# Performance work log

Measured on AMD Instinct MI355X. Metric: run time of the kernel, lower is better.

## Reference

```python
import jax, jax.numpy as jnp
import numpy as np

THETA = 10.0  # gaussian sharpness from __init__


def _bilinear_align_corners(x, out_h, out_w):
    # torch F.interpolate(mode='bilinear', align_corners=True)
    n, c, H, W = x.shape
    ys = jnp.arange(out_h, dtype=x.dtype) * ((H - 1) / (out_h - 1))
    xs = jnp.arange(out_w, dtype=x.dtype) * ((W - 1) / (out_w - 1))
    y0 = jnp.floor(ys).astype(jnp.int32)
    y1 = jnp.minimum(y0 + 1, H - 1)
    wy = ys - y0.astype(x.dtype)
    x0 = jnp.floor(xs).astype(jnp.int32)
    x1 = jnp.minimum(x0 + 1, W - 1)
    wx = xs - x0.astype(x.dtype)
    top = x[:, :, y0, :]
    bot = x[:, :, y1, :]
    xh = top * (1 - wy)[None, None, :, None] + bot * wy[None, None, :, None]
    left = xh[:, :, :, x0]
    right = xh[:, :, :, x1]
    return left * (1 - wx)[None, None, None, :] + right * wx[None, None, None, :]


def _unfold3x3(x):
    # torch F.unfold(kernel_size=3, padding=1, stride=1).view(n, c, 9, h, w)
    # zero padding; kernel positions in row-major order
    n, c, h, w = x.shape
    p = jnp.pad(x, ((0, 0), (0, 0), (1, 1), (1, 1)))
    patches = [p[:, :, di:di + h, dj:dj + w] for di in range(3) for dj in range(3)]
    return jnp.stack(patches, axis=2)  # [n, c, 9, h, w]


def reference(mask, edge):
    n, c, h, w = mask.shape
    e = _bilinear_align_corners(edge, h, w)          # [n, 1, h, w]
    le = e[:, :, None] - _unfold3x3(e)               # [n, 1, 9, h, w]
    wgt = jax.nn.softmax(-THETA * le * le, axis=2)   # gaussian similarity softmax over 3x3 nbhd
    m = _unfold3x3(mask) * wgt                       # [n, c, 9, h, w]
    return m.sum(axis=2)                             # [n, c, h, w]


def setup_inputs() -> dict:
    key = jax.random.key(0)
    k1, k2 = jax.random.split(key)
    mask = jax.random.normal(k1, (8, 64, 128, 128), dtype=jnp.float32)
    edge = jax.random.normal(k2, (8, 1, 64, 64), dtype=jnp.float32)
    return {"mask": mask, "edge": edge}
```

## Files before the change

### kernel.cpp

```cpp
#include <hip/hip_runtime.h>


#define THETA 10.0f

constexpr int NB = 8;
constexpr int C  = 64;
constexpr int H  = 128, W = 128;
constexpr int EH = 64,  EW = 64;

constexpr int ROWS = 8;
constexpr int CG   = 8;

typedef float f4v __attribute__((ext_vector_type(4)));

__global__ __launch_bounds__(256) void geg_kernel(
    const float* __restrict__ mask,
    const float* __restrict__ edge,
    float* __restrict__ out)
{
    __shared__ float e_s[ROWS + 2][W + 4];

    const int t     = threadIdx.x;
    const int cg    = blockIdx.x;
    const int ytile = blockIdx.y;
    const int n     = blockIdx.z;
    const int y0    = ytile * ROWS;

    const int lane = t & 31;
    const int x4   = lane * 4;
    const int r    = t >> 5;
    const int gy   = y0 + r;

    int rowoff[3];
    rowoff[0] = max(gy - 1, 0) * W + x4;
    rowoff[1] = gy * W + x4;
    rowoff[2] = min(gy + 1, H - 1) * W + x4;

    const int c0 = cg * CG;
    const float* mptr = mask + (size_t)(n * C + c0) * (H * W);

    float4 buf[2][3];
    #pragma unroll
    for (int i = 0; i < 3; ++i) {
        buf[0][i] = *(const float4*)(mptr + rowoff[i]);
        buf[1][i] = *(const float4*)(mptr + H * W + rowoff[i]);
    }

    const float* eg = edge + n * (EH * EW);
    const float s = 63.0f / 127.0f;
    const int rr0 = t >> 7;
    const int cc0 = t & 127;
    #pragma unroll
    for (int rb = 0; rb < ROWS + 2; rb += 2) {
        const int rr = rb + rr0;
        for (int cc = cc0; cc < W + 2; cc += 128) {
            int egy = y0 - 1 + rr;
            int egx = cc - 1;
            float v = 0.0f;
            if (egy >= 0 && egy < H && egx >= 0 && egx < W) {
                float ys = egy * s;
                float xs = egx * s;
                float yf = floorf(ys), xf = floorf(xs);
                int iy0 = (int)yf, ix0 = (int)xf;
                int iy1 = min(iy0 + 1, EH - 1), ix1 = min(ix0 + 1, EW - 1);
                float wy = ys - yf, wx = xs - xf;
                float tl = eg[iy0 * EW + ix0], tr = eg[iy0 * EW + ix1];
                float bl = eg[iy1 * EW + ix0], br = eg[iy1 * EW + ix1];
                float lv = tl + (bl - tl) * wy;
                float rv = tr + (br - tr) * wy;
                v = lv + (rv - lv) * wx;
            }
            e_s[rr][cc] = v;
        }
    }
    __syncthreads();

    float w[4][9];
    #pragma unroll
    for (int p = 0; p < 4; ++p) {
        const int gx = x4 + p;
        const float c = e_s[r + 1][gx + 1];
        float a[9], sum = 0.0f;
        #pragma unroll
        for (int di = 0; di < 3; ++di) {
            #pragma unroll
            for (int dj = 0; dj < 3; ++dj) {
                float d = c - e_s[r + di][gx + dj];
                float e = __expf(-THETA * d * d);
                a[di * 3 + dj] = e;
                sum += e;
            }
        }
        const float inv = 1.0f / sum;
        #pragma unroll
        for (int di = 0; di < 3; ++di) {
            #pragma unroll
            for (int dj = 0; dj < 3; ++dj) {
                int ny = gy + di - 1, nx = gx + dj - 1;
                bool ok = (ny >= 0) & (ny < H) & (nx >= 0) & (nx < W);
                w[p][di * 3 + dj] = ok ? a[di * 3 + dj] * inv : 0.0f;
            }
        }
    }

    float* optr = out + (size_t)(n * C + c0) * (H * W) + gy * W + x4;

    #pragma unroll
    for (int ci = 0; ci < CG; ++ci) {
        float4 cur[3];
        #pragma unroll
        for (int i = 0; i < 3; ++i) cur[i] = buf[ci & 1][i];

        if (ci + 2 < CG) {
            #pragma unroll
            for (int i = 0; i < 3; ++i)
                buf[ci & 1][i] = *(const float4*)(mptr + (ci + 2) * (H * W) + rowoff[i]);
        }

        float av[4] = {0.f, 0.f, 0.f, 0.f};
        #pragma unroll
        for (int i = 0; i < 3; ++i) {
            float m6[6];
            m6[0] = __shfl_up(cur[i].w, 1, 32);
            m6[1] = cur[i].x; m6[2] = cur[i].y; m6[3] = cur[i].z; m6[4] = cur[i].w;
            m6[5] = __shfl_down(cur[i].x, 1, 32);
            #pragma unroll
            for (int p = 0; p < 4; ++p) {
                av[p] = fmaf(m6[p + 0], w[p][i * 3 + 0],
                        fmaf(m6[p + 1], w[p][i * 3 + 1],
                        fmaf(m6[p + 2], w[p][i * 3 + 2], av[p])));
            }
        }
        f4v v; v.x = av[0]; v.y = av[1]; v.z = av[2]; v.w = av[3];
        __builtin_nontemporal_store(v, (f4v*)(optr + ci * (H * W)));
    }
}

extern "C" void kernel_launch(void* const* d_in, const int* in_sizes, int n_in,
                              void* d_out, int out_size, void* d_ws, size_t ws_size,
                              hipStream_t stream) {
    const float* mask = (const float*)d_in[0];
    const float* edge = (const float*)d_in[1];
    float* out = (float*)d_out;

    dim3 grid(C / CG, H / ROWS, NB);
    dim3 block(256);
    geg_kernel<<<grid, block, 0, stream>>>(mask, edge, out);
}
```

Measured before the change: 85.93 us.

## Remap threads to 2 pixels each with full-wave rows and 4-row tiles

Each thread now handles 2 adjacent pixels instead of 4, so one 64-lane wavefront covers a full 128-pixel row, and the block covers 4 rows instead of 8. This doubles the grid, lowers per-thread register use and adds an occupancy hint to launch_bounds, all aimed at more memory-level parallelism. In exchange, loads become float2, the edge halo is recomputed proportionally more often, and the nontemporal store is replaced by a plain float2 store. The shuffles now use the full wave width.

```diff
diff --git a/kernel.cpp b/kernel.cpp
--- a/kernel.cpp
+++ b/kernel.cpp
@@ -7,13 +7,12 @@
 constexpr int C  = 64;
 constexpr int H  = 128, W = 128;
 constexpr int EH = 64,  EW = 64;
+constexpr int HW = H * W;
 
-constexpr int ROWS = 8;
+constexpr int ROWS = 4;
 constexpr int CG   = 8;
 
-typedef float f4v __attribute__((ext_vector_type(4)));
-
-__global__ __launch_bounds__(256) void geg_kernel(
+__global__ __launch_bounds__(256, 8) void geg_kernel(
     const float* __restrict__ mask,
     const float* __restrict__ edge,
     float* __restrict__ out)
@@ -26,24 +25,24 @@
     const int n     = blockIdx.z;
     const int y0    = ytile * ROWS;
 
-    const int lane = t & 31;
-    const int x4   = lane * 4;
-    const int r    = t >> 5;
+    const int lane = t & 63;
+    const int x2   = lane * 2;
+    const int r    = t >> 6;
     const int gy   = y0 + r;
 
     int rowoff[3];
-    rowoff[0] = max(gy - 1, 0) * W + x4;
-    rowoff[1] = gy * W + x4;
-    rowoff[2] = min(gy + 1, H - 1) * W + x4;
+    rowoff[0] = max(gy - 1, 0) * W + x2;
+    rowoff[1] = gy * W + x2;
+    rowoff[2] = min(gy + 1, H - 1) * W + x2;
 
     const int c0 = cg * CG;
-    const float* mptr = mask + (size_t)(n * C + c0) * (H * W);
+    const float* mptr = mask + (size_t)(n * C + c0) * HW;
 
-    float4 buf[2][3];
+    float2 buf[2][3];
     #pragma unroll
     for (int i = 0; i < 3; ++i) {
-        buf[0][i] = *(const float4*)(mptr + rowoff[i]);
-        buf[1][i] = *(const float4*)(mptr + H * W + rowoff[i]);
+        buf[0][i] = *(const float2*)(mptr + rowoff[i]);
+        buf[1][i] = *(const float2*)(mptr + HW + rowoff[i]);
     }
 
     const float* eg = edge + n * (EH * EW);
@@ -75,10 +74,10 @@
     }
     __syncthreads();
 
-    float w[4][9];
+    float w[2][9];
     #pragma unroll
-    for (int p = 0; p < 4; ++p) {
-        const int gx = x4 + p;
+    for (int p = 0; p < 2; ++p) {
+        const int gx = x2 + p;
         const float c = e_s[r + 1][gx + 1];
         float a[9], sum = 0.0f;
         #pragma unroll
@@ -103,36 +102,35 @@
         }
     }
 
-    float* optr = out + (size_t)(n * C + c0) * (H * W) + gy * W + x4;
+    float* optr = out + (size_t)(n * C + c0) * HW + gy * W + x2;
 
     #pragma unroll
     for (int ci = 0; ci < CG; ++ci) {
-        float4 cur[3];
+        float2 cur[3];
         #pragma unroll
         for (int i = 0; i < 3; ++i) cur[i] = buf[ci & 1][i];
 
         if (ci + 2 < CG) {
             #pragma unroll
             for (int i = 0; i < 3; ++i)
-                buf[ci & 1][i] = *(const float4*)(mptr + (ci + 2) * (H * W) + rowoff[i]);
+                buf[ci & 1][i] = *(const float2*)(mptr + (ci + 2) * HW + rowoff[i]);
         }
 
-        float av[4] = {0.f, 0.f, 0.f, 0.f};
+        float av[2] = {0.f, 0.f};
         #pragma unroll
         for (int i = 0; i < 3; ++i) {
-            float m6[6];
-            m6[0] = __shfl_up(cur[i].w, 1, 32);
-            m6[1] = cur[i].x; m6[2] = cur[i].y; m6[3] = cur[i].z; m6[4] = cur[i].w;
-            m6[5] = __shfl_down(cur[i].x, 1, 32);
+            float m4[4];
+            m4[0] = __shfl_up(cur[i].y, 1);
+            m4[1] = cur[i].x; m4[2] = cur[i].y;
+            m4[3] = __shfl_down(cur[i].x, 1);
             #pragma unroll
-            for (int p = 0; p < 4; ++p) {
-                av[p] = fmaf(m6[p + 0], w[p][i * 3 + 0],
-                        fmaf(m6[p + 1], w[p][i * 3 + 1],
-                        fmaf(m6[p + 2], w[p][i * 3 + 2], av[p])));
+            for (int p = 0; p < 2; ++p) {
+                av[p] = fmaf(m4[p + 0], w[p][i * 3 + 0],
+                        fmaf(m4[p + 1], w[p][i * 3 + 1],
+                        fmaf(m4[p + 2], w[p][i * 3 + 2], av[p])));
             }
         }
-        f4v v; v.x = av[0]; v.y = av[1]; v.z = av[2]; v.w = av[3];
-        __builtin_nontemporal_store(v, (f4v*)(optr + ci * (H * W)));
+        *(float2*)(optr + ci * HW) = make_float2(av[0], av[1]);
     }
 }
 
```

New measurement: 86.89 us. No clear change (+1.1%).
